# Kernel optimization log

Hardware: AMD Instinct MI355X
Metric: run time of the kernel (lower is better)

The kernel has to match this reference:

```python
import jax, jax.numpy as jnp
import numpy as np


def _pairwise_sq_dists(p, t):
    # p: [N,3], t: [M,3] -> [N,M] squared euclidean distances
    # |p|^2 + |t|^2 - 2 p.t^T (avoids materializing [N,M,3])
    p2 = jnp.sum(p * p, axis=-1)  # [N]
    t2 = jnp.sum(t * t, axis=-1)  # [M]
    cross = jnp.einsum('nd,md->nm', p, t)  # [N,M]
    d = p2[:, None] + t2[None, :] - 2.0 * cross
    return jnp.maximum(d, 0.0)  # clamp tiny negatives from cancellation


def setup_inputs() -> dict:
    key = jax.random.key(0)
    k1, k2 = jax.random.split(key)
    N = 16384
    predict = jax.random.normal(k1, (1, N, 3), dtype=jnp.float32)
    target = jax.random.normal(k2, (1, N, 3), dtype=jnp.float32)
    return {"predict": predict, "target": target}


def reference(predict, target):
    # Faithful to forward: only the first batch element is used.
    p = predict[0]  # [N,3]
    t = target[0]   # [M,3]
    d = _pairwise_sq_dists(p, t)          # [N,M] squared distances
    dist1 = jnp.min(d, axis=1)            # nearest target for each predict pt
    dist2 = jnp.min(d, axis=0)            # nearest predict for each target pt
    loss = jnp.mean(dist1) + jnp.mean(dist2)
    return loss
```

## Files before the change

kernel.cpp:

```cpp
#include <hip/hip_runtime.h>


typedef short s16x8 __attribute__((ext_vector_type(8)));
typedef float f32x16 __attribute__((ext_vector_type(16)));

static __device__ __forceinline__ unsigned short f2bf(float f) {
    unsigned u = __float_as_uint(f);
    unsigned r = (u + 0x7FFFu + ((u >> 16) & 1u)) >> 16;
    return (unsigned short)r;
}
static __device__ __forceinline__ float bf2f(unsigned short h) {
    return __uint_as_float(((unsigned)h) << 16);
}
static __device__ __forceinline__ void split2(float v, unsigned short& h, unsigned short& l) {
    h = f2bf(v);
    l = f2bf(v - bf2f(h));
}

union Pack16 { unsigned short u[16]; uint4 v[2]; };

__global__ void prep_pack(const float* __restrict__ predict, const float* __restrict__ target,
                          unsigned short* __restrict__ ApP, unsigned short* __restrict__ BpP,
                          unsigned short* __restrict__ ApT, unsigned short* __restrict__ BpT,
                          unsigned* __restrict__ ticket, int N)
{
    int i = blockIdx.x * blockDim.x + threadIdx.x;
    if (i == 0) *ticket = 0u;
    if (i >= 2 * N) return;
    const float* src = (i < N) ? predict : target;
    unsigned short* Ap = (i < N) ? ApP : ApT;
    unsigned short* Bp = (i < N) ? BpP : BpT;
    int j = (i < N) ? i : i - N;

    float x = src[3*j], y = src[3*j+1], z = src[3*j+2];
    float n2 = __builtin_fmaf(x, x, __builtin_fmaf(y, y, z*z));

    unsigned short xh,xl,yh,yl,zh,zl,nh,nl,qxh,qxl,qyh,qyl,qzh,qzl;
    split2(x, xh, xl); split2(y, yh, yl); split2(z, zh, zl); split2(n2, nh, nl);
    split2(-2.0f*x, qxh, qxl); split2(-2.0f*y, qyh, qyl); split2(-2.0f*z, qzh, qzl);
    const unsigned short one = f2bf(1.0f);

    Pack16 a, b;
    a.u[0]=xh; a.u[1]=xh; a.u[2]=xl; a.u[3]=xl;
    a.u[4]=yh; a.u[5]=yh; a.u[6]=yl; a.u[7]=yl;
    a.u[8]=zh; a.u[9]=zh; a.u[10]=zl; a.u[11]=zl;
    a.u[12]=nh; a.u[13]=nl; a.u[14]=one; a.u[15]=one;

    b.u[0]=qxh; b.u[1]=qxl; b.u[2]=qxh; b.u[3]=qxl;
    b.u[4]=qyh; b.u[5]=qyl; b.u[6]=qyh; b.u[7]=qyl;
    b.u[8]=qzh; b.u[9]=qzl; b.u[10]=qzh; b.u[11]=qzl;
    b.u[12]=one; b.u[13]=one; b.u[14]=nh; b.u[15]=nl;

    uint4* ad = (uint4*)(Ap + (size_t)j * 16);
    uint4* bd = (uint4*)(Bp + (size_t)j * 16);
    ad[0] = a.v[0]; ad[1] = a.v[1];
    bd[0] = b.v[0]; bd[1] = b.v[1];
}

#define CG 8
#define RB 32

__global__ __launch_bounds__(256, 4) void chamfer_main(
    const unsigned short* __restrict__ ApP, const unsigned short* __restrict__ BpP,
    const unsigned short* __restrict__ ApT, const unsigned short* __restrict__ BpT,
    float* __restrict__ partials, int N)
{
    const int dir = blockIdx.z;
    const unsigned short* __restrict__ Ap = dir ? ApT : ApP;
    const unsigned short* __restrict__ Bp = dir ? BpP : BpT;
    float* __restrict__ pout = partials + (size_t)(dir * CG + blockIdx.y) * N;

    const int tid  = threadIdx.x;
    const int w    = tid >> 6;
    const int lane = tid & 63;
    const int lm   = lane & 31;
    const int lg   = lane >> 5;

    const int row0 = blockIdx.x * 256 + w * 64;

    const uint4* A4 = (const uint4*)Ap;
    s16x8 a0 = __builtin_bit_cast(s16x8, A4[(size_t)(row0      + lm) * 2 + lg]);
    s16x8 a1 = __builtin_bit_cast(s16x8, A4[(size_t)(row0 + 32 + lm) * 2 + lg]);

    float rm0[16], rm1[16];
    #pragma unroll
    for (int r = 0; r < 16; ++r) { rm0[r] = 3.0e38f; rm1[r] = 3.0e38f; }

    const f32x16 zc = {0.f,0.f,0.f,0.f,0.f,0.f,0.f,0.f,0.f,0.f,0.f,0.f,0.f,0.f,0.f,0.f};

    const int npt = N / CG;
    const int NT  = npt / 32;
    const uint4* bp = (const uint4*)Bp + (size_t)blockIdx.y * npt * 2 + lm * 2 + lg;

    uint4 c0 = bp[0];
    uint4 c1 = bp[64];
    const uint4* bnext = bp + 128;

    for (int t = 0; t < NT - 2; t += 2) {
        uint4 n0 = bnext[0];
        uint4 n1 = bnext[64];
        bnext += 128;
        s16x8 bA = __builtin_bit_cast(s16x8, c0);
        s16x8 bB = __builtin_bit_cast(s16x8, c1);
        f32x16 p0 = __builtin_amdgcn_mfma_f32_32x32x16_bf16(a0, bA, zc, 0, 0, 0);
        f32x16 q0 = __builtin_amdgcn_mfma_f32_32x32x16_bf16(a0, bB, zc, 0, 0, 0);
        f32x16 p1 = __builtin_amdgcn_mfma_f32_32x32x16_bf16(a1, bA, zc, 0, 0, 0);
        f32x16 q1 = __builtin_amdgcn_mfma_f32_32x32x16_bf16(a1, bB, zc, 0, 0, 0);
        #pragma unroll
        for (int r = 0; r < 16; ++r) {
            rm0[r] = fminf(fminf(rm0[r], p0[r]), q0[r]);
            rm1[r] = fminf(fminf(rm1[r], p1[r]), q1[r]);
        }
        c0 = n0; c1 = n1;
    }
    {
        s16x8 bA = __builtin_bit_cast(s16x8, c0);
        s16x8 bB = __builtin_bit_cast(s16x8, c1);
        f32x16 p0 = __builtin_amdgcn_mfma_f32_32x32x16_bf16(a0, bA, zc, 0, 0, 0);
        f32x16 q0 = __builtin_amdgcn_mfma_f32_32x32x16_bf16(a0, bB, zc, 0, 0, 0);
        f32x16 p1 = __builtin_amdgcn_mfma_f32_32x32x16_bf16(a1, bA, zc, 0, 0, 0);
        f32x16 q1 = __builtin_amdgcn_mfma_f32_32x32x16_bf16(a1, bB, zc, 0, 0, 0);
        #pragma unroll
        for (int r = 0; r < 16; ++r) {
            rm0[r] = fminf(fminf(rm0[r], p0[r]), q0[r]);
            rm1[r] = fminf(fminf(rm1[r], p1[r]), q1[r]);
        }
    }

    #pragma unroll
    for (int m = 1; m <= 16; m <<= 1) {
        #pragma unroll
        for (int r = 0; r < 16; ++r) {
            rm0[r] = fminf(rm0[r], __shfl_xor(rm0[r], m, 64));
            rm1[r] = fminf(rm1[r], __shfl_xor(rm1[r], m, 64));
        }
    }
    #pragma unroll
    for (int r = 0; r < 16; ++r) {
        int rl = (r & 3) + 8 * (r >> 2) + 4 * lg;
        if (lm == r) {
            pout[row0 +      rl] = rm0[r];
            pout[row0 + 32 + rl] = rm1[r];
        }
    }
}

__global__ void chamfer_reduce(const float* __restrict__ partials,
                               double* __restrict__ bsum, unsigned* __restrict__ ticket,
                               float* __restrict__ out, int N)
{
    const int n4 = N >> 2;
    const float4* p4 = (const float4*)partials;
    double acc = 0.0;
    for (int i = blockIdx.x * blockDim.x + threadIdx.x; i < n4;
         i += gridDim.x * blockDim.x) {
        float4 m0 = p4[i];
        #pragma unroll
        for (int g = 1; g < CG; ++g) {
            float4 v = p4[(size_t)g * n4 + i];
            m0.x = fminf(m0.x, v.x); m0.y = fminf(m0.y, v.y);
            m0.z = fminf(m0.z, v.z); m0.w = fminf(m0.w, v.w);
        }
        float4 m1 = p4[(size_t)CG * n4 + i];
        #pragma unroll
        for (int g = CG + 1; g < 2 * CG; ++g) {
            float4 v = p4[(size_t)g * n4 + i];
            m1.x = fminf(m1.x, v.x); m1.y = fminf(m1.y, v.y);
            m1.z = fminf(m1.z, v.z); m1.w = fminf(m1.w, v.w);
        }
        acc += (double)fmaxf(m0.x, 0.0f) + (double)fmaxf(m0.y, 0.0f)
             + (double)fmaxf(m0.z, 0.0f) + (double)fmaxf(m0.w, 0.0f)
             + (double)fmaxf(m1.x, 0.0f) + (double)fmaxf(m1.y, 0.0f)
             + (double)fmaxf(m1.z, 0.0f) + (double)fmaxf(m1.w, 0.0f);
    }
    for (int off = 32; off; off >>= 1)
        acc += __shfl_down(acc, off, 64);
    __shared__ double sacc[4];
    const int wave = threadIdx.x >> 6, lane = threadIdx.x & 63;
    if (lane == 0) sacc[wave] = acc;
    __syncthreads();

    __shared__ unsigned is_last;
    if (threadIdx.x == 0) {
        bsum[blockIdx.x] = sacc[0] + sacc[1] + sacc[2] + sacc[3];
        __threadfence();
        unsigned old = atomicAdd(ticket, 1u);
        is_last = (old == gridDim.x - 1u) ? 1u : 0u;
    }
    __syncthreads();
    if (!is_last) return;

    if (threadIdx.x == 0) {
        __threadfence();
        double t = 0.0;
        for (int i = 0; i < RB; ++i) t += bsum[i];
        out[0] = (float)(t / (double)N);
    }
}

extern "C" void kernel_launch(void* const* d_in, const int* in_sizes, int n_in,
                              void* d_out, int out_size, void* d_ws, size_t ws_size,
                              hipStream_t stream) {
    const float* predict = (const float*)d_in[0];
    const float* target  = (const float*)d_in[1];
    const int N = in_sizes[0] / 3;

    unsigned short* ws16 = (unsigned short*)d_ws;
    unsigned short* ApP = ws16;
    unsigned short* BpP = ws16 + (size_t)1 * N * 16;
    unsigned short* ApT = ws16 + (size_t)2 * N * 16;
    unsigned short* BpT = ws16 + (size_t)3 * N * 16;
    float* partials = (float*)(ws16 + (size_t)4 * N * 16);
    double* bsum = (double*)(partials + (size_t)2 * CG * N);
    unsigned* ticket = (unsigned*)(bsum + RB);

    prep_pack<<<dim3((2 * N + 255) / 256), dim3(256), 0, stream>>>(
        predict, target, ApP, BpP, ApT, BpT, ticket, N);

    dim3 grid(N / 256, CG, 2);
    chamfer_main<<<grid, dim3(256), 0, stream>>>(ApP, BpP, ApT, BpT, partials, N);

    chamfer_reduce<<<dim3(RB), dim3(256), 0, stream>>>(
        partials, bsum, ticket, (float*)d_out, N);
}
```

Measured before the change: 83.21 us.

## Compute both Chamfer directions from a single distance-matrix pass

The kernel now evaluates the N×M distance tiles once and takes both row minima (kept in registers) and column minima (reduced across the MFMA tile and stored per wave in shared memory). This removes the second direction's full MFMA pass and its repacked operands. The column-group count is raised to keep the grid size the same. In exchange, each tile needs extra VALU min work and cross-lane shuffles. It also writes a much larger column-partial buffer (64 row-blocks × N) that the reduce kernel must scan, so reduction traffic grows.

```diff
diff --git a/kernel.cpp b/kernel.cpp
--- a/kernel.cpp
+++ b/kernel.cpp
@@ -16,67 +16,74 @@
     h = f2bf(v);
     l = f2bf(v - bf2f(h));
 }
+static __device__ __forceinline__ float colmin16(f32x16 v) {
+    float a = fminf(v[0], v[1]),  b = fminf(v[2], v[3]);
+    float c = fminf(v[4], v[5]),  d = fminf(v[6], v[7]);
+    float e = fminf(v[8], v[9]),  f = fminf(v[10], v[11]);
+    float g = fminf(v[12], v[13]), h = fminf(v[14], v[15]);
+    return fminf(fminf(fminf(a, b), fminf(c, d)),
+                 fminf(fminf(e, f), fminf(g, h)));
+}
 
 union Pack16 { unsigned short u[16]; uint4 v[2]; };
 
+#define CG  16
+#define NRB 64
+#define RB  32
+
 __global__ void prep_pack(const float* __restrict__ predict, const float* __restrict__ target,
-                          unsigned short* __restrict__ ApP, unsigned short* __restrict__ BpP,
-                          unsigned short* __restrict__ ApT, unsigned short* __restrict__ BpT,
+                          unsigned short* __restrict__ ApP, unsigned short* __restrict__ BpT,
                           unsigned* __restrict__ ticket, int N)
 {
     int i = blockIdx.x * blockDim.x + threadIdx.x;
     if (i == 0) *ticket = 0u;
     if (i >= 2 * N) return;
-    const float* src = (i < N) ? predict : target;
-    unsigned short* Ap = (i < N) ? ApP : ApT;
-    unsigned short* Bp = (i < N) ? BpP : BpT;
-    int j = (i < N) ? i : i - N;
-
-    float x = src[3*j], y = src[3*j+1], z = src[3*j+2];
-    float n2 = __builtin_fmaf(x, x, __builtin_fmaf(y, y, z*z));
-
-    unsigned short xh,xl,yh,yl,zh,zl,nh,nl,qxh,qxl,qyh,qyl,qzh,qzl;
-    split2(x, xh, xl); split2(y, yh, yl); split2(z, zh, zl); split2(n2, nh, nl);
-    split2(-2.0f*x, qxh, qxl); split2(-2.0f*y, qyh, qyl); split2(-2.0f*z, qzh, qzl);
     const unsigned short one = f2bf(1.0f);
 
-    Pack16 a, b;
-    a.u[0]=xh; a.u[1]=xh; a.u[2]=xl; a.u[3]=xl;
-    a.u[4]=yh; a.u[5]=yh; a.u[6]=yl; a.u[7]=yl;
-    a.u[8]=zh; a.u[9]=zh; a.u[10]=zl; a.u[11]=zl;
-    a.u[12]=nh; a.u[13]=nl; a.u[14]=one; a.u[15]=one;
-
-    b.u[0]=qxh; b.u[1]=qxl; b.u[2]=qxh; b.u[3]=qxl;
-    b.u[4]=qyh; b.u[5]=qyl; b.u[6]=qyh; b.u[7]=qyl;
-    b.u[8]=qzh; b.u[9]=qzl; b.u[10]=qzh; b.u[11]=qzl;
-    b.u[12]=one; b.u[13]=one; b.u[14]=nh; b.u[15]=nl;
-
-    uint4* ad = (uint4*)(Ap + (size_t)j * 16);
-    uint4* bd = (uint4*)(Bp + (size_t)j * 16);
-    ad[0] = a.v[0]; ad[1] = a.v[1];
-    bd[0] = b.v[0]; bd[1] = b.v[1];
-}
-
-#define CG 8
-#define RB 32
+    if (i < N) {
+        float x = predict[3*i], y = predict[3*i+1], z = predict[3*i+2];
+        float n2 = __builtin_fmaf(x, x, __builtin_fmaf(y, y, z*z));
+        unsigned short xh,xl,yh,yl,zh,zl,nh,nl;
+        split2(x, xh, xl); split2(y, yh, yl); split2(z, zh, zl); split2(n2, nh, nl);
+        Pack16 a;
+        a.u[0]=xh; a.u[1]=xh; a.u[2]=xl; a.u[3]=xl;
+        a.u[4]=yh; a.u[5]=yh; a.u[6]=yl; a.u[7]=yl;
+        a.u[8]=zh; a.u[9]=zh; a.u[10]=zl; a.u[11]=zl;
+        a.u[12]=nh; a.u[13]=nl; a.u[14]=one; a.u[15]=one;
+        uint4* ad = (uint4*)(ApP + (size_t)i * 16);
+        ad[0] = a.v[0]; ad[1] = a.v[1];
+    } else {
+        int j = i - N;
+        float x = target[3*j], y = target[3*j+1], z = target[3*j+2];
+        float n2 = __builtin_fmaf(x, x, __builtin_fmaf(y, y, z*z));
+        unsigned short nh,nl,qxh,qxl,qyh,qyl,qzh,qzl;
+        split2(n2, nh, nl);
+        split2(-2.0f*x, qxh, qxl); split2(-2.0f*y, qyh, qyl); split2(-2.0f*z, qzh, qzl);
+        Pack16 b;
+        b.u[0]=qxh; b.u[1]=qxl; b.u[2]=qxh; b.u[3]=qxl;
+        b.u[4]=qyh; b.u[5]=qyl; b.u[6]=qyh; b.u[7]=qyl;
+        b.u[8]=qzh; b.u[9]=qzl; b.u[10]=qzh; b.u[11]=qzl;
+        b.u[12]=one; b.u[13]=one; b.u[14]=nh; b.u[15]=nl;
+        uint4* bd = (uint4*)(BpT + (size_t)j * 16);
+        bd[0] = b.v[0]; bd[1] = b.v[1];
+    }
+}
 
 __global__ __launch_bounds__(256, 4) void chamfer_main(
-    const unsigned short* __restrict__ ApP, const unsigned short* __restrict__ BpP,
-    const unsigned short* __restrict__ ApT, const unsigned short* __restrict__ BpT,
-    float* __restrict__ partials, int N)
+    const unsigned short* __restrict__ Ap, const unsigned short* __restrict__ Bp,
+    float* __restrict__ partials1, float* __restrict__ cpart, int N)
 {
-    const int dir = blockIdx.z;
-    const unsigned short* __restrict__ Ap = dir ? ApT : ApP;
-    const unsigned short* __restrict__ Bp = dir ? BpP : BpT;
-    float* __restrict__ pout = partials + (size_t)(dir * CG + blockIdx.y) * N;
+    __shared__ float cm[4][1024];
 
     const int tid  = threadIdx.x;
     const int w    = tid >> 6;
     const int lane = tid & 63;
     const int lm   = lane & 31;
     const int lg   = lane >> 5;
-
-    const int row0 = blockIdx.x * 256 + w * 64;
+    const int bx   = blockIdx.x;
+    const int cg   = blockIdx.y;
+
+    const int row0 = bx * 256 + w * 64;
 
     const uint4* A4 = (const uint4*)Ap;
     s16x8 a0 = __builtin_bit_cast(s16x8, A4[(size_t)(row0      + lm) * 2 + lg]);
@@ -90,42 +97,46 @@
 
     const int npt = N / CG;
     const int NT  = npt / 32;
-    const uint4* bp = (const uint4*)Bp + (size_t)blockIdx.y * npt * 2 + lm * 2 + lg;
+    const uint4* bp = (const uint4*)Bp + (size_t)cg * npt * 2 + lm * 2 + lg;
+    float* cmw = cm[w];
 
     uint4 c0 = bp[0];
     uint4 c1 = bp[64];
     const uint4* bnext = bp + 128;
 
-    for (int t = 0; t < NT - 2; t += 2) {
+#define BODY(TT)                                                              \
+    {                                                                         \
+        s16x8 bA = __builtin_bit_cast(s16x8, c0);                             \
+        s16x8 bB = __builtin_bit_cast(s16x8, c1);                             \
+        f32x16 p0 = __builtin_amdgcn_mfma_f32_32x32x16_bf16(a0, bA, zc, 0,0,0);\
+        f32x16 q0 = __builtin_amdgcn_mfma_f32_32x32x16_bf16(a0, bB, zc, 0,0,0);\
+        f32x16 p1 = __builtin_amdgcn_mfma_f32_32x32x16_bf16(a1, bA, zc, 0,0,0);\
+        f32x16 q1 = __builtin_amdgcn_mfma_f32_32x32x16_bf16(a1, bB, zc, 0,0,0);\
+        _Pragma("unroll")                                                     \
+        for (int r = 0; r < 16; ++r) {                                        \
+            rm0[r] = fminf(fminf(rm0[r], p0[r]), q0[r]);                      \
+            rm1[r] = fminf(fminf(rm1[r], p1[r]), q1[r]);                      \
+        }                                                                     \
+        float va = fminf(colmin16(p0), colmin16(p1));                         \
+        va = fminf(va, __shfl_xor(va, 32, 64));                               \
+        float vb = fminf(colmin16(q0), colmin16(q1));                         \
+        vb = fminf(vb, __shfl_xor(vb, 32, 64));                               \
+        if (lane < 32) {                                                      \
+            cmw[(TT) * 32 + lm]      = va;                                    \
+            cmw[(TT) * 32 + 32 + lm] = vb;                                    \
+        }                                                                     \
+    }
+
+    int t = 0;
+    for (; t < NT - 2; t += 2) {
         uint4 n0 = bnext[0];
         uint4 n1 = bnext[64];
         bnext += 128;
-        s16x8 bA = __builtin_bit_cast(s16x8, c0);
-        s16x8 bB = __builtin_bit_cast(s16x8, c1);
-        f32x16 p0 = __builtin_amdgcn_mfma_f32_32x32x16_bf16(a0, bA, zc, 0, 0, 0);
-        f32x16 q0 = __builtin_amdgcn_mfma_f32_32x32x16_bf16(a0, bB, zc, 0, 0, 0);
-        f32x16 p1 = __builtin_amdgcn_mfma_f32_32x32x16_bf16(a1, bA, zc, 0, 0, 0);
-        f32x16 q1 = __builtin_amdgcn_mfma_f32_32x32x16_bf16(a1, bB, zc, 0, 0, 0);
-        #pragma unroll
-        for (int r = 0; r < 16; ++r) {
-            rm0[r] = fminf(fminf(rm0[r], p0[r]), q0[r]);
-            rm1[r] = fminf(fminf(rm1[r], p1[r]), q1[r]);
-        }
+        BODY(t);
         c0 = n0; c1 = n1;
     }
-    {
-        s16x8 bA = __builtin_bit_cast(s16x8, c0);
-        s16x8 bB = __builtin_bit_cast(s16x8, c1);
-        f32x16 p0 = __builtin_amdgcn_mfma_f32_32x32x16_bf16(a0, bA, zc, 0, 0, 0);
-        f32x16 q0 = __builtin_amdgcn_mfma_f32_32x32x16_bf16(a0, bB, zc, 0, 0, 0);
-        f32x16 p1 = __builtin_amdgcn_mfma_f32_32x32x16_bf16(a1, bA, zc, 0, 0, 0);
-        f32x16 q1 = __builtin_amdgcn_mfma_f32_32x32x16_bf16(a1, bB, zc, 0, 0, 0);
-        #pragma unroll
-        for (int r = 0; r < 16; ++r) {
-            rm0[r] = fminf(fminf(rm0[r], p0[r]), q0[r]);
-            rm1[r] = fminf(fminf(rm1[r], p1[r]), q1[r]);
-        }
-    }
+    BODY(t);
+#undef BODY
 
     #pragma unroll
     for (int m = 1; m <= 16; m <<= 1) {
@@ -135,6 +146,7 @@
             rm1[r] = fminf(rm1[r], __shfl_xor(rm1[r], m, 64));
         }
     }
+    float* __restrict__ pout = partials1 + (size_t)cg * N;
     #pragma unroll
     for (int r = 0; r < 16; ++r) {
         int rl = (r & 3) + 8 * (r >> 2) + 4 * lg;
@@ -143,35 +155,44 @@
             pout[row0 + 32 + rl] = rm1[r];
         }
     }
-}
-
-__global__ void chamfer_reduce(const float* __restrict__ partials,
+
+    __syncthreads();
+    float* __restrict__ crow = cpart + (size_t)bx * N + (size_t)cg * npt;
+    for (int c = tid; c < npt; c += 256) {
+        float m = fminf(fminf(cm[0][c], cm[1][c]), fminf(cm[2][c], cm[3][c]));
+        crow[c] = m;
+    }
+}
+
+__global__ void chamfer_reduce(const float* __restrict__ partials1,
+                               const float* __restrict__ cpart,
                                double* __restrict__ bsum, unsigned* __restrict__ ticket,
                                float* __restrict__ out, int N)
 {
     const int n4 = N >> 2;
-    const float4* p4 = (const float4*)partials;
+    const float4* p4 = (const float4*)partials1;
+    const float4* c4 = (const float4*)cpart;
     double acc = 0.0;
     for (int i = blockIdx.x * blockDim.x + threadIdx.x; i < n4;
          i += gridDim.x * blockDim.x) {
-        float4 m0 = p4[i];
+        float4 m = p4[i];
         #pragma unroll
         for (int g = 1; g < CG; ++g) {
             float4 v = p4[(size_t)g * n4 + i];
-            m0.x = fminf(m0.x, v.x); m0.y = fminf(m0.y, v.y);
-            m0.z = fminf(m0.z, v.z); m0.w = fminf(m0.w, v.w);
-        }
-        float4 m1 = p4[(size_t)CG * n4 + i];
-        #pragma unroll
-        for (int g = CG + 1; g < 2 * CG; ++g) {
-            float4 v = p4[(size_t)g * n4 + i];
-            m1.x = fminf(m1.x, v.x); m1.y = fminf(m1.y, v.y);
-            m1.z = fminf(m1.z, v.z); m1.w = fminf(m1.w, v.w);
-        }
-        acc += (double)fmaxf(m0.x, 0.0f) + (double)fmaxf(m0.y, 0.0f)
-             + (double)fmaxf(m0.z, 0.0f) + (double)fmaxf(m0.w, 0.0f)
-             + (double)fmaxf(m1.x, 0.0f) + (double)fmaxf(m1.y, 0.0f)
-             + (double)fmaxf(m1.z, 0.0f) + (double)fmaxf(m1.w, 0.0f);
+            m.x = fminf(m.x, v.x); m.y = fminf(m.y, v.y);
+            m.z = fminf(m.z, v.z); m.w = fminf(m.w, v.w);
+        }
+        acc += (double)fmaxf(m.x, 0.0f) + (double)fmaxf(m.y, 0.0f)
+             + (double)fmaxf(m.z, 0.0f) + (double)fmaxf(m.w, 0.0f);
+
+        float4 mc = c4[i];
+        for (int g = 1; g < NRB; ++g) {
+            float4 v = c4[(size_t)g * n4 + i];
+            mc.x = fminf(mc.x, v.x); mc.y = fminf(mc.y, v.y);
+            mc.z = fminf(mc.z, v.z); mc.w = fminf(mc.w, v.w);
+        }
+        acc += (double)fmaxf(mc.x, 0.0f) + (double)fmaxf(mc.y, 0.0f)
+             + (double)fmaxf(mc.z, 0.0f) + (double)fmaxf(mc.w, 0.0f);
     }
     for (int off = 32; off; off >>= 1)
         acc += __shfl_down(acc, off, 64);
@@ -207,19 +228,18 @@
 
     unsigned short* ws16 = (unsigned short*)d_ws;
     unsigned short* ApP = ws16;
-    unsigned short* BpP = ws16 + (size_t)1 * N * 16;
-    unsigned short* ApT = ws16 + (size_t)2 * N * 16;
-    unsigned short* BpT = ws16 + (size_t)3 * N * 16;
-    float* partials = (float*)(ws16 + (size_t)4 * N * 16);
-    double* bsum = (double*)(partials + (size_t)2 * CG * N);
+    unsigned short* BpT = ws16 + (size_t)1 * N * 16;
+    float* partials1 = (float*)(ws16 + (size_t)2 * N * 16);
+    float* cpart = partials1 + (size_t)CG * N;
+    double* bsum = (double*)(cpart + (size_t)NRB * N);
     unsigned* ticket = (unsigned*)(bsum + RB);
 
     prep_pack<<<dim3((2 * N + 255) / 256), dim3(256), 0, stream>>>(
-        predict, target, ApP, BpP, ApT, BpT, ticket, N);
-
-    dim3 grid(N / 256, CG, 2);
-    chamfer_main<<<grid, dim3(256), 0, stream>>>(ApP, BpP, ApT, BpT, partials, N);
+        predict, target, ApP, BpT, ticket, N);
+
+    dim3 grid(N / 256, CG);
+    chamfer_main<<<grid, dim3(256), 0, stream>>>(ApP, BpT, partials1, cpart, N);
 
     chamfer_reduce<<<dim3(RB), dim3(256), 0, stream>>>(
-        partials, bsum, ticket, (float*)d_out, N);
-}
+        partials1, cpart, bsum, ticket, (float*)d_out, N);
+}
```

Measured after the change: 93.03 us. +11.8%, slower.
